# Kernel optimization log

Measured on AMD Instinct MI355X. Metric: run time of the kernel, lower is better.

## Reference

```python
import jax, jax.numpy as jnp
import numpy as np

N, C, H, W = 16, 128, 112, 112
P, HG, WG = 98, 16, 16  # 98 patches, 16x16 sample grid each


def setup_inputs() -> dict:
    key = jax.random.key(0)
    k1, k2 = jax.random.split(key)
    feature_maps = jax.random.normal(k1, (N, C, H, W), dtype=jnp.float32)
    # grid_sample normalized coords in [-1, 1]
    meshgrid = jax.random.uniform(k2, (N, P, HG, WG, 2), dtype=jnp.float32) * 2.0 - 1.0
    return {"feature_maps": feature_maps, "meshgrid": meshgrid}


def _grid_sample_bilinear_border(fm, grid):
    # fm: [N, C, H, W]; grid: [N, P, Hg, Wg, 2] (x, y) in [-1, 1]
    # torch grid_sample(mode='bilinear', padding_mode='border', align_corners=False)
    n, c, h, w = fm.shape
    gx, gy = grid[..., 0], grid[..., 1]
    # unnormalize (align_corners=False) then clamp to border
    x = jnp.clip((gx + 1.0) * (w * 0.5) - 0.5, 0.0, w - 1.0)
    y = jnp.clip((gy + 1.0) * (h * 0.5) - 0.5, 0.0, h - 1.0)
    x0 = jnp.floor(x)
    y0 = jnp.floor(y)
    wx = x - x0  # [N, P, Hg, Wg]
    wy = y - y0
    x0i = jnp.clip(x0.astype(jnp.int32), 0, w - 1)
    x1i = jnp.clip(x0i + 1, 0, w - 1)
    y0i = jnp.clip(y0.astype(jnp.int32), 0, h - 1)
    y1i = jnp.clip(y0i + 1, 0, h - 1)
    b = jnp.arange(n).reshape(n, 1, 1, 1)
    gather = lambda yi, xi: fm[b, :, yi, xi]  # -> [N, P, Hg, Wg, C]
    out = (gather(y0i, x0i) * ((1.0 - wy) * (1.0 - wx))[..., None]
           + gather(y0i, x1i) * ((1.0 - wy) * wx)[..., None]
           + gather(y1i, x0i) * (wy * (1.0 - wx))[..., None]
           + gather(y1i, x1i) * (wy * wx)[..., None])
    # [N, P, Hg, Wg, C] -> [N, P, C, Hg, Wg]
    return jnp.moveaxis(out, -1, 2)


def reference(feature_maps, meshgrid):
    # Single fused batched sample over all 98 patches (equivalent to the
    # torch loop of 98 grid_sample calls + stack + permute(1,0,2,3,4)).
    return _grid_sample_bilinear_border(feature_maps, meshgrid)
```

## Files before the change

### kernel.cpp

```cpp
#include <hip/hip_runtime.h>
#include <hip/hip_fp16.h>


#define NN 16
#define CC 128
#define HH 112
#define WW 112
#define PP 98
#define PTS 256
#define NPTS (PP * PTS)
#define NQUADS (NPTS / 4)
#define HWs (HH * WW)
#define PAD 113
#define THREADS 512

typedef float f32x4 __attribute__((ext_vector_type(4)));
typedef unsigned int u32x4 __attribute__((ext_vector_type(4)));

__device__ __forceinline__ unsigned int pack2(float a, float b) {
  __half2 h = __floats2half2_rn(a, b);
  return *reinterpret_cast<unsigned int*>(&h);
}

__device__ __forceinline__ float2 samp(const unsigned int* __restrict__ plane,
                                       float gx, float gy) {
  const float x = fminf(fmaxf(fmaf(gx, (float)WW * 0.5f, (float)WW * 0.5f - 0.5f),
                              0.0f), (float)(WW - 1));
  const float y = fminf(fmaxf(fmaf(gy, (float)HH * 0.5f, (float)HH * 0.5f - 0.5f),
                              0.0f), (float)(HH - 1));
  const float x0f = floorf(x), y0f = floorf(y);
  const float wx = x - x0f, wy = y - y0f;
  const unsigned int* p0 = reinterpret_cast<const unsigned int*>(
      reinterpret_cast<const char*>(plane) + ((int)y0f * WW + (int)x0f) * 4);
  const __half2 h00 = *reinterpret_cast<const __half2*>(&p0[0]);
  const __half2 h01 = *reinterpret_cast<const __half2*>(&p0[1]);
  const __half2 h10 = *reinterpret_cast<const __half2*>(&p0[WW]);
  const __half2 h11 = *reinterpret_cast<const __half2*>(&p0[WW + 1]);
  const float2 f00 = __half22float2(h00);
  const float2 f01 = __half22float2(h01);
  const float2 f10 = __half22float2(h10);
  const float2 f11 = __half22float2(h11);
  const float ux = 1.0f - wx, uy = 1.0f - wy;
  const float w00 = uy * ux, w01 = uy * wx, w10 = wy * ux, w11 = wy * wx;
  float2 r;
  r.x = fmaf(f11.x, w11, fmaf(f10.x, w10, fmaf(f01.x, w01, f00.x * w00)));
  r.y = fmaf(f11.y, w11, fmaf(f10.y, w10, fmaf(f01.y, w01, f00.y * w00)));
  return r;
}

__global__ __launch_bounds__(THREADS) void patches_kernel(
    const float* __restrict__ fm,
    const float* __restrict__ grid,
    float* __restrict__ out) {
  __shared__ unsigned int plane[HWs + PAD];

  const int n = blockIdx.y;
  const int t = threadIdx.x;
  const f32x4* __restrict__ g4 =
      reinterpret_cast<const f32x4*>(grid + (size_t)n * NPTS * 2);

  for (int half = 0; half < 2; ++half) {
    const int cp = blockIdx.x * 2 + half;
    const int c0 = cp * 2;

    if (half) __syncthreads();

    const f32x4* __restrict__ srcA =
        reinterpret_cast<const f32x4*>(fm + ((size_t)n * CC + c0) * HWs);
    const f32x4* __restrict__ srcB =
        reinterpret_cast<const f32x4*>(fm + ((size_t)n * CC + c0 + 1) * HWs);
    u32x4* dst = reinterpret_cast<u32x4*>(plane);
    for (int i = t; i < HWs / 4; i += THREADS) {
      const f32x4 a = __builtin_nontemporal_load(&srcA[i]);
      const f32x4 b = __builtin_nontemporal_load(&srcB[i]);
      u32x4 q;
      q.x = pack2(a.x, b.x);
      q.y = pack2(a.y, b.y);
      q.z = pack2(a.z, b.z);
      q.w = pack2(a.w, b.w);
      dst[i] = q;
    }
    if (t < PAD) plane[HWs + t] = 0u;
    __syncthreads();

    float* __restrict__ obase = out + ((size_t)n * PP * CC + c0) * PTS;

#pragma unroll 2
    for (int it = 0; it < 13; ++it) {
      const int q = t + it * THREADS;
      if (q < NQUADS) {
        const f32x4 ga = g4[q * 2];
        const f32x4 gb = g4[q * 2 + 1];
        const float2 r0 = samp(plane, ga.x, ga.y);
        const float2 r1 = samp(plane, ga.z, ga.w);
        const float2 r2 = samp(plane, gb.x, gb.y);
        const float2 r3 = samp(plane, gb.z, gb.w);
        f32x4 vA, vB;
        vA.x = r0.x; vA.y = r1.x; vA.z = r2.x; vA.w = r3.x;
        vB.x = r0.y; vB.y = r1.y; vB.z = r2.y; vB.w = r3.y;
        const int p = q >> 6;
        const int s4 = (q & 63) * 4;
        float* o = obase + (size_t)p * CC * PTS + s4;
        __builtin_nontemporal_store(vA, reinterpret_cast<f32x4*>(o));
        __builtin_nontemporal_store(vB, reinterpret_cast<f32x4*>(o + PTS));
      }
    }
  }
}

extern "C" void kernel_launch(void* const* d_in, const int* in_sizes, int n_in,
                              void* d_out, int out_size, void* d_ws, size_t ws_size,
                              hipStream_t stream) {
  const float* fm = (const float*)d_in[0];
  const float* grid = (const float*)d_in[1];
  float* out = (float*)d_out;

  dim3 grd(CC / 4, NN);
  dim3 blk(THREADS);
  patches_kernel<<<grd, blk, 0, stream>>>(fm, grid, out);
}
```

Measured before the change: 283.2 us.

## Double-buffer channel-pair planes in LDS and overlap loads with sampling

Each block now handles four channel pairs instead of two and keeps two LDS plane buffers. The next pair's global loads go into registers while the current pair is sampled, then get written to the other buffer, so feature-map load latency overlaps with gather compute. It also moves to 1024-thread blocks and a 256-block 1D grid, remapped so each XCD sees the same batch images and grid data. The trade-offs are half as many blocks, twice the LDS per block (about 100KB, so likely only one block per CU), and higher register pressure from the eight staged vectors.

```diff
diff --git a/kernel.cpp b/kernel.cpp
--- a/kernel.cpp
+++ b/kernel.cpp
@@ -11,8 +11,9 @@
 #define NPTS (PP * PTS)
 #define NQUADS (NPTS / 4)
 #define HWs (HH * WW)
+#define HW4 (HWs / 4)
 #define PAD 113
-#define THREADS 512
+#define THREADS 1024
 
 typedef float f32x4 __attribute__((ext_vector_type(4)));
 typedef unsigned int u32x4 __attribute__((ext_vector_type(4)));
@@ -48,53 +49,74 @@
   return r;
 }
 
-__global__ __launch_bounds__(THREADS) void patches_kernel(
+__global__ __launch_bounds__(THREADS, 4) void patches_kernel(
     const float* __restrict__ fm,
     const float* __restrict__ grid,
     float* __restrict__ out) {
-  __shared__ unsigned int plane[HWs + PAD];
+  __shared__ unsigned int lbuf[2][HWs + PAD];
 
-  const int n = blockIdx.y;
+  const int b = blockIdx.x;
+  const int xcd = b & 7;
+  const int idx = b >> 3;
+  const int n = (xcd << 1) | (idx >> 4);
+  const int cpb = (idx & 15) * 4;
   const int t = threadIdx.x;
+
   const f32x4* __restrict__ g4 =
       reinterpret_cast<const f32x4*>(grid + (size_t)n * NPTS * 2);
 
-  for (int half = 0; half < 2; ++half) {
-    const int cp = blockIdx.x * 2 + half;
-    const int c0 = cp * 2;
+  if (t < PAD) { lbuf[0][HWs + t] = 0u; lbuf[1][HWs + t] = 0u; }
 
-    if (half) __syncthreads();
+  f32x4 ra0, ra1, ra2, ra3, rb0, rb1, rb2, rb3;
 
-    const f32x4* __restrict__ srcA =
-        reinterpret_cast<const f32x4*>(fm + ((size_t)n * CC + c0) * HWs);
-    const f32x4* __restrict__ srcB =
-        reinterpret_cast<const f32x4*>(fm + ((size_t)n * CC + c0 + 1) * HWs);
-    u32x4* dst = reinterpret_cast<u32x4*>(plane);
-    for (int i = t; i < HWs / 4; i += THREADS) {
-      const f32x4 a = __builtin_nontemporal_load(&srcA[i]);
-      const f32x4 b = __builtin_nontemporal_load(&srcB[i]);
-      u32x4 q;
-      q.x = pack2(a.x, b.x);
-      q.y = pack2(a.y, b.y);
-      q.z = pack2(a.z, b.z);
-      q.w = pack2(a.w, b.w);
-      dst[i] = q;
+  auto stage_load = [&](int j) {
+    const f32x4* __restrict__ sA = reinterpret_cast<const f32x4*>(
+        fm + ((size_t)n * CC + (size_t)(cpb + j) * 2) * HWs);
+    const f32x4* __restrict__ sB = sA + HW4;
+    ra0 = __builtin_nontemporal_load(&sA[t]);
+    ra1 = __builtin_nontemporal_load(&sA[t + 1024]);
+    ra2 = __builtin_nontemporal_load(&sA[t + 2048]);
+    rb0 = __builtin_nontemporal_load(&sB[t]);
+    rb1 = __builtin_nontemporal_load(&sB[t + 1024]);
+    rb2 = __builtin_nontemporal_load(&sB[t + 2048]);
+    if (t < HW4 - 3072) {
+      ra3 = __builtin_nontemporal_load(&sA[t + 3072]);
+      rb3 = __builtin_nontemporal_load(&sB[t + 3072]);
     }
-    if (t < PAD) plane[HWs + t] = 0u;
-    __syncthreads();
+  };
 
-    float* __restrict__ obase = out + ((size_t)n * PP * CC + c0) * PTS;
+  auto stage_write = [&](unsigned int* d) {
+    u32x4* dst = reinterpret_cast<u32x4*>(d);
+    u32x4 q;
+    q.x = pack2(ra0.x, rb0.x); q.y = pack2(ra0.y, rb0.y);
+    q.z = pack2(ra0.z, rb0.z); q.w = pack2(ra0.w, rb0.w);
+    dst[t] = q;
+    q.x = pack2(ra1.x, rb1.x); q.y = pack2(ra1.y, rb1.y);
+    q.z = pack2(ra1.z, rb1.z); q.w = pack2(ra1.w, rb1.w);
+    dst[t + 1024] = q;
+    q.x = pack2(ra2.x, rb2.x); q.y = pack2(ra2.y, rb2.y);
+    q.z = pack2(ra2.z, rb2.z); q.w = pack2(ra2.w, rb2.w);
+    dst[t + 2048] = q;
+    if (t < HW4 - 3072) {
+      q.x = pack2(ra3.x, rb3.x); q.y = pack2(ra3.y, rb3.y);
+      q.z = pack2(ra3.z, rb3.z); q.w = pack2(ra3.w, rb3.w);
+      dst[t + 3072] = q;
+    }
+  };
 
+  auto compute = [&](int j, const unsigned int* __restrict__ pl) {
+    float* __restrict__ obase =
+        out + ((size_t)n * PP * CC + (size_t)(cpb + j) * 2) * PTS;
 #pragma unroll 2
-    for (int it = 0; it < 13; ++it) {
-      const int q = t + it * THREADS;
+    for (int it = 0; it < 7; ++it) {
+      const int q = t + it * 1024;
       if (q < NQUADS) {
         const f32x4 ga = g4[q * 2];
         const f32x4 gb = g4[q * 2 + 1];
-        const float2 r0 = samp(plane, ga.x, ga.y);
-        const float2 r1 = samp(plane, ga.z, ga.w);
-        const float2 r2 = samp(plane, gb.x, gb.y);
-        const float2 r3 = samp(plane, gb.z, gb.w);
+        const float2 r0 = samp(pl, ga.x, ga.y);
+        const float2 r1 = samp(pl, ga.z, ga.w);
+        const float2 r2 = samp(pl, gb.x, gb.y);
+        const float2 r3 = samp(pl, gb.z, gb.w);
         f32x4 vA, vB;
         vA.x = r0.x; vA.y = r1.x; vA.z = r2.x; vA.w = r3.x;
         vB.x = r0.y; vB.y = r1.y; vB.z = r2.y; vB.w = r3.y;
@@ -105,6 +127,17 @@
         __builtin_nontemporal_store(vB, reinterpret_cast<f32x4*>(o + PTS));
       }
     }
+  };
+
+  stage_load(0);
+  stage_write(lbuf[0]);
+  __syncthreads();
+#pragma unroll 1
+  for (int j = 0; j < 4; ++j) {
+    if (j < 3) stage_load(j + 1);
+    compute(j, lbuf[j & 1]);
+    if (j < 3) stage_write(lbuf[(j + 1) & 1]);
+    __syncthreads();
   }
 }
 
@@ -115,7 +148,7 @@
   const float* grid = (const float*)d_in[1];
   float* out = (float*)d_out;
 
-  dim3 grd(CC / 4, NN);
+  dim3 grd(256);
   dim3 blk(THREADS);
   patches_kernel<<<grd, blk, 0, stream>>>(fm, grid, out);
 }
```

Result: slower. 293.1 us (+3.5%).

## Prefetch next channel pair into registers during sampling and remap blocks by XCD

Applied to the files above, without the earlier changes.

Loads the second channel pair's feature planes into registers before computing the first pair, so the global reads overlap the sampling and store phase. The grid becomes 1D, and the block index is decoded so that blocks for the same batch image land on the same XCD, aiming for better L2 reuse of the sampling grid. The cost is higher register pressure: 14 float4 registers held across compute, which may lower occupancy or spill.

```diff
diff --git a/kernel.cpp b/kernel.cpp
--- a/kernel.cpp
+++ b/kernel.cpp
@@ -11,8 +11,10 @@
 #define NPTS (PP * PTS)
 #define NQUADS (NPTS / 4)
 #define HWs (HH * WW)
+#define HW4 (HWs / 4)
 #define PAD 113
 #define THREADS 512
+#define CHUNKS 6
 
 typedef float f32x4 __attribute__((ext_vector_type(4)));
 typedef unsigned int u32x4 __attribute__((ext_vector_type(4)));
@@ -54,37 +56,57 @@
     float* __restrict__ out) {
   __shared__ unsigned int plane[HWs + PAD];
 
-  const int n = blockIdx.y;
+  const int b = blockIdx.x;
+  const int xcd = b & 7;
+  const int i = b >> 3;
+  const int n = xcd * 2 + (i >> 5);
+  const int cpg = i & 31;
   const int t = threadIdx.x;
+
   const f32x4* __restrict__ g4 =
       reinterpret_cast<const f32x4*>(grid + (size_t)n * NPTS * 2);
 
-  for (int half = 0; half < 2; ++half) {
-    const int cp = blockIdx.x * 2 + half;
-    const int c0 = cp * 2;
+  f32x4 ra[CHUNKS + 1], rb[CHUNKS + 1];
 
-    if (half) __syncthreads();
+  auto load_pair = [&](int cp) {
+    const f32x4* __restrict__ sA = reinterpret_cast<const f32x4*>(
+        fm + ((size_t)n * CC + (size_t)cp * 2) * HWs);
+    const f32x4* __restrict__ sB = sA + HW4;
+#pragma unroll
+    for (int k = 0; k < CHUNKS; ++k) {
+      ra[k] = __builtin_nontemporal_load(&sA[t + k * THREADS]);
+      rb[k] = __builtin_nontemporal_load(&sB[t + k * THREADS]);
+    }
+    if (t < HW4 - CHUNKS * THREADS) {
+      ra[CHUNKS] = __builtin_nontemporal_load(&sA[t + CHUNKS * THREADS]);
+      rb[CHUNKS] = __builtin_nontemporal_load(&sB[t + CHUNKS * THREADS]);
+    }
+  };
 
-    const f32x4* __restrict__ srcA =
-        reinterpret_cast<const f32x4*>(fm + ((size_t)n * CC + c0) * HWs);
-    const f32x4* __restrict__ srcB =
-        reinterpret_cast<const f32x4*>(fm + ((size_t)n * CC + c0 + 1) * HWs);
+  auto write_pair = [&]() {
     u32x4* dst = reinterpret_cast<u32x4*>(plane);
-    for (int i = t; i < HWs / 4; i += THREADS) {
-      const f32x4 a = __builtin_nontemporal_load(&srcA[i]);
-      const f32x4 b = __builtin_nontemporal_load(&srcB[i]);
+#pragma unroll
+    for (int k = 0; k < CHUNKS; ++k) {
       u32x4 q;
-      q.x = pack2(a.x, b.x);
-      q.y = pack2(a.y, b.y);
-      q.z = pack2(a.z, b.z);
-      q.w = pack2(a.w, b.w);
-      dst[i] = q;
+      q.x = pack2(ra[k].x, rb[k].x);
+      q.y = pack2(ra[k].y, rb[k].y);
+      q.z = pack2(ra[k].z, rb[k].z);
+      q.w = pack2(ra[k].w, rb[k].w);
+      dst[t + k * THREADS] = q;
     }
-    if (t < PAD) plane[HWs + t] = 0u;
-    __syncthreads();
+    if (t < HW4 - CHUNKS * THREADS) {
+      u32x4 q;
+      q.x = pack2(ra[CHUNKS].x, rb[CHUNKS].x);
+      q.y = pack2(ra[CHUNKS].y, rb[CHUNKS].y);
+      q.z = pack2(ra[CHUNKS].z, rb[CHUNKS].z);
+      q.w = pack2(ra[CHUNKS].w, rb[CHUNKS].w);
+      dst[t + CHUNKS * THREADS] = q;
+    }
+  };
 
-    float* __restrict__ obase = out + ((size_t)n * PP * CC + c0) * PTS;
-
+  auto compute = [&](int cp) {
+    float* __restrict__ obase =
+        out + ((size_t)n * PP * CC + (size_t)cp * 2) * PTS;
 #pragma unroll 2
     for (int it = 0; it < 13; ++it) {
       const int q = t + it * THREADS;
@@ -105,7 +127,21 @@
         __builtin_nontemporal_store(vB, reinterpret_cast<f32x4*>(o + PTS));
       }
     }
-  }
+  };
+
+  const int cp0 = cpg * 2, cp1 = cpg * 2 + 1;
+
+  load_pair(cp0);
+  if (t < PAD) plane[HWs + t] = 0u;
+  write_pair();
+  load_pair(cp1);
+  __builtin_amdgcn_sched_barrier(0);
+  __syncthreads();
+  compute(cp0);
+  __syncthreads();
+  write_pair();
+  __syncthreads();
+  compute(cp1);
 }
 
 extern "C" void kernel_launch(void* const* d_in, const int* in_sizes, int n_in,
@@ -115,7 +151,7 @@
   const float* grid = (const float*)d_in[1];
   float* out = (float*)d_out;
 
-  dim3 grd(CC / 4, NN);
+  dim3 grd(512);
   dim3 blk(THREADS);
   patches_kernel<<<grd, blk, 0, stream>>>(fm, grid, out);
 }
```

After: 288.2 us. About the same (+1.8%).
